# Kernel optimization log

Hardware: AMD Instinct MI355X
Metric: run time of the kernel (lower is better)

## Reference

```python
import jax, jax.numpy as jnp
import numpy as np

B, T, D, H, Q = 8, 1024, 256, 4, 3
DK = D // H


def _ln(x, g, b):
    m = x.mean(-1, keepdims=True)
    v = x.var(-1, keepdims=True)
    return (x - m) / jnp.sqrt(v + 1e-5) * g + b


def _grn(x, f1w, f1b, f2w, f2b, gw, gb, lng, lnb):
    # GatedResidualNetwork (input_size == output_size, dropout in eval mode)
    eta1 = jax.nn.elu(x @ f1w.T + f1b)
    eta2 = eta1 @ f2w.T + f2b
    a = jax.nn.sigmoid(eta2 @ gw.T + gb) * eta2
    return _ln(x + a, lng, lnb)


def setup_inputs() -> dict:
    key = jax.random.key(0)
    ks = jax.random.split(key, 24)
    s = 0.02
    p = {}
    p['x'] = jax.random.normal(ks[0], (B, T, D), dtype=jnp.float32)
    # GRN 1 (temporal enrichment before attention)
    p['g1_f1w'] = jax.random.normal(ks[1], (D, D)) * s
    p['g1_f1b'] = jnp.zeros((D,))
    p['g1_f2w'] = jax.random.normal(ks[2], (D, D)) * s
    p['g1_f2b'] = jnp.zeros((D,))
    p['g1_gw'] = jax.random.normal(ks[3], (D, D)) * s
    p['g1_gb'] = jnp.zeros((D,))
    p['g1_lng'] = jnp.ones((D,))
    p['g1_lnb'] = jnp.zeros((D,))
    # Multi-head self-attention
    p['wq'] = jax.random.normal(ks[4], (D, D)) * s
    p['wk'] = jax.random.normal(ks[5], (D, D)) * s
    p['wv'] = jax.random.normal(ks[6], (D, D)) * s
    p['wo_w'] = jax.random.normal(ks[7], (D, D)) * s
    p['wo_b'] = jnp.zeros((D,))
    p['attn_lng'] = jnp.ones((D,))
    p['attn_lnb'] = jnp.zeros((D,))
    # GRN 2 (post-attention gating)
    p['g2_f1w'] = jax.random.normal(ks[8], (D, D)) * s
    p['g2_f1b'] = jnp.zeros((D,))
    p['g2_f2w'] = jax.random.normal(ks[9], (D, D)) * s
    p['g2_f2b'] = jnp.zeros((D,))
    p['g2_gw'] = jax.random.normal(ks[10], (D, D)) * s
    p['g2_gb'] = jnp.zeros((D,))
    p['g2_lng'] = jnp.ones((D,))
    p['g2_lnb'] = jnp.zeros((D,))
    # Quantile heads: Linear(D -> Q)
    p['qh_w'] = jax.random.normal(ks[11], (Q, D)) * s
    p['qh_b'] = jnp.zeros((Q,))
    return p


def reference(x, g1_f1w, g1_f1b, g1_f2w, g1_f2b, g1_gw, g1_gb, g1_lng, g1_lnb,
              wq, wk, wv, wo_w, wo_b, attn_lng, attn_lnb,
              g2_f1w, g2_f1b, g2_f2w, g2_f2b, g2_gw, g2_gb, g2_lng, g2_lnb,
              qh_w, qh_b):
    b, t, d = x.shape
    h = _grn(x, g1_f1w, g1_f1b, g1_f2w, g1_f2b, g1_gw, g1_gb, g1_lng, g1_lnb)
    # self-attention (W_q/W_k/W_v have no bias, per module)
    q = (h @ wq.T).reshape(b, t, H, DK)
    k = (h @ wk.T).reshape(b, t, H, DK)
    v = (h @ wv.T).reshape(b, t, H, DK)
    scale = 1.0 / np.sqrt(DK).astype(np.float32)
    scores = jnp.einsum('bthd,bshd->bhts', q, k) * scale  # [B,H,T,T]
    attn = jax.nn.softmax(scores, axis=-1)
    ctx = jnp.einsum('bhts,bshd->bthd', attn, v).reshape(b, t, d)
    attn_out = ctx @ wo_w.T + wo_b
    h2 = _ln(h + attn_out, attn_lng, attn_lnb)
    h3 = _grn(h2, g2_f1w, g2_f1b, g2_f2w, g2_f2b, g2_gw, g2_gb, g2_lng, g2_lnb)
    # quantile heads on the last decoder step (CUDAQuantileHeadsFunction: [B,D]->[B,Q])
    out = h3[:, -1, :] @ qh_w.T + qh_b  # [B, Q]
    return out
```

## Files before the change

### kernel.cpp

```cpp
#include <hip/hip_runtime.h>
#include <hip/hip_bf16.h>
#include <math.h>

#define DD 256
#define BB 8
#define TT 1024
#define MM (BB*TT)
#define NH 4
#define DKH 64
#define NQ 3

typedef __attribute__((ext_vector_type(8))) short bf16x8;
typedef __attribute__((ext_vector_type(4))) float f32x4;
typedef unsigned short u16;
typedef unsigned int u32;

__device__ __forceinline__ float bf2f(u16 u) {
  return __uint_as_float(((u32)u) << 16);
}
__device__ __forceinline__ u16 f2bf(float x) {
  __hip_bfloat16 h = __float2bfloat16(x);
  return *reinterpret_cast<u16*>(&h);
}
__device__ __forceinline__ uint2 pack4(float a, float b, float c, float d) {
  uint2 r;
  r.x = (u32)f2bf(a) | ((u32)f2bf(b) << 16);
  r.y = (u32)f2bf(c) | ((u32)f2bf(d) << 16);
  return r;
}
__device__ __forceinline__ float wred(float v) {
#pragma unroll
  for (int off = 32; off; off >>= 1) v += __shfl_xor(v, off);
  return v;
}

#define NX8 (MM * DD / 8)
#define NW8 (65536 / 8)
#define NCHUNK (NX8 + 9 * NW8)

__global__ __launch_bounds__(256) void precast(
    const float* __restrict__ x,
    const float* __restrict__ w0, const float* __restrict__ w1,
    const float* __restrict__ w2, const float* __restrict__ w3,
    const float* __restrict__ w4, const float* __restrict__ w5,
    const float* __restrict__ w6, const float* __restrict__ w7,
    const float* __restrict__ w8_, u16* __restrict__ wb,
    u16* __restrict__ xb)
{
  const int c = blockIdx.x * 256 + threadIdx.x;
  if (c >= NCHUNK) return;
  const float* src;
  u16* dst;
  int off;
  if (c < NX8) {
    src = x; dst = xb; off = c * 8;
  } else {
    const int r = c - NX8;
    const int mi = r / NW8;
    off = (r - mi * NW8) * 8;
    switch (mi) {
      case 0: src = w0; break; case 1: src = w1; break;
      case 2: src = w2; break; case 3: src = w3; break;
      case 4: src = w4; break; case 5: src = w5; break;
      case 6: src = w6; break; case 7: src = w7; break;
      default: src = w8_; break;
    }
    dst = wb + mi * 65536;
  }
  const float4 v0 = *(const float4*)(src + off);
  const float4 v1 = *(const float4*)(src + off + 4);
  *(uint2*)(dst + off)     = pack4(v0.x, v0.y, v0.z, v0.w);
  *(uint2*)(dst + off + 4) = pack4(v1.x, v1.y, v1.z, v1.w);
}

template<int ACT>
__global__ __launch_bounds__(256) void gemm64(const u16* __restrict__ A_,
                                              const u16* __restrict__ W,
                                              const float* __restrict__ bias,
                                              u16* __restrict__ out)
{
  __shared__ u16 As[64][264];
  __shared__ u16 Bs[64][264];
  const int tid  = threadIdx.x;
  const int lane = tid & 63, wave = tid >> 6;
  const int wr = wave >> 1, wc = wave & 1;
  const int q  = lane >> 4, lr = lane & 15;
  const int m0 = blockIdx.x * 64, n0 = blockIdx.y * 64;

#pragma unroll
  for (int p = 0; p < 8; ++p) {
    const int c = tid + p * 256;
    const int row = c >> 5, col = (c & 31) * 8;
    *(uint4*)&As[row][col] = *(const uint4*)(A_ + (size_t)(m0 + row) * DD + col);
    *(uint4*)&Bs[row][col] = *(const uint4*)(W  + (size_t)(n0 + row) * DD + col);
  }
  __syncthreads();

  f32x4 acc[2][2] = {};
#pragma unroll
  for (int kk = 0; kk < 8; ++kk) {
    const int koff = kk * 32 + q * 8;
    bf16x8 av[2], bv[2];
    av[0] = *(const bf16x8*)&As[wr * 32 + lr][koff];
    av[1] = *(const bf16x8*)&As[wr * 32 + 16 + lr][koff];
    bv[0] = *(const bf16x8*)&Bs[wc * 32 + lr][koff];
    bv[1] = *(const bf16x8*)&Bs[wc * 32 + 16 + lr][koff];
#pragma unroll
    for (int i = 0; i < 2; ++i)
#pragma unroll
      for (int j = 0; j < 2; ++j)
        acc[i][j] = __builtin_amdgcn_mfma_f32_16x16x32_bf16(av[i], bv[j], acc[i][j], 0, 0, 0);
  }

#pragma unroll
  for (int i = 0; i < 2; ++i) {
#pragma unroll
    for (int j = 0; j < 2; ++j) {
      const int col = n0 + wc * 32 + j * 16 + lr;
      const float bvv = bias ? bias[col] : 0.f;
#pragma unroll
      for (int t = 0; t < 4; ++t) {
        const int row = m0 + wr * 32 + i * 16 + q * 4 + t;
        float v = acc[i][j][t] + bvv;
        if (ACT == 1) v = v > 0.f ? v : expm1f(v);
        out[(size_t)row * DD + col] = f2bf(v);
      }
    }
  }
}

__global__ __launch_bounds__(256) void gemm_kv(const u16* __restrict__ A_,
                                               const u16* __restrict__ Wk,
                                               const u16* __restrict__ Wv,
                                               u16* __restrict__ kout,
                                               u16* __restrict__ vout)
{
  __shared__ u16 As[64][264];
  __shared__ u16 Bs[64][264];
  const int tid  = threadIdx.x;
  const int lane = tid & 63, wave = tid >> 6;
  const int wr = wave >> 1, wc = wave & 1;
  const int q  = lane >> 4, lr = lane & 15;
  const int ny = blockIdx.y;
  const u16* W = (ny < 4) ? Wk : Wv;
  u16* out = (ny < 4) ? kout : vout;
  const int m0 = blockIdx.x * 64, n0 = (ny & 3) * 64;

#pragma unroll
  for (int p = 0; p < 8; ++p) {
    const int c = tid + p * 256;
    const int row = c >> 5, col = (c & 31) * 8;
    *(uint4*)&As[row][col] = *(const uint4*)(A_ + (size_t)(m0 + row) * DD + col);
    *(uint4*)&Bs[row][col] = *(const uint4*)(W  + (size_t)(n0 + row) * DD + col);
  }
  __syncthreads();

  f32x4 acc[2][2] = {};
#pragma unroll
  for (int kk = 0; kk < 8; ++kk) {
    const int koff = kk * 32 + q * 8;
    bf16x8 av[2], bv[2];
    av[0] = *(const bf16x8*)&As[wr * 32 + lr][koff];
    av[1] = *(const bf16x8*)&As[wr * 32 + 16 + lr][koff];
    bv[0] = *(const bf16x8*)&Bs[wc * 32 + lr][koff];
    bv[1] = *(const bf16x8*)&Bs[wc * 32 + 16 + lr][koff];
#pragma unroll
    for (int i = 0; i < 2; ++i)
#pragma unroll
      for (int j = 0; j < 2; ++j)
        acc[i][j] = __builtin_amdgcn_mfma_f32_16x16x32_bf16(av[i], bv[j], acc[i][j], 0, 0, 0);
  }

#pragma unroll
  for (int i = 0; i < 2; ++i) {
#pragma unroll
    for (int j = 0; j < 2; ++j) {
      const int col = n0 + wc * 32 + j * 16 + lr;
#pragma unroll
      for (int t = 0; t < 4; ++t) {
        const int row = m0 + wr * 32 + i * 16 + q * 4 + t;
        out[(size_t)row * DD + col] = f2bf(acc[i][j][t]);
      }
    }
  }
}

__global__ __launch_bounds__(256) void grn_gate_ln(
    const u16* __restrict__ eta2, const u16* __restrict__ W,
    const float* __restrict__ gb, const float* __restrict__ x,
    const float* __restrict__ lng, const float* __restrict__ lnb,
    u16* __restrict__ hout, float* __restrict__ hlast)
{
  __shared__ u16 As[32][136];
  __shared__ u16 Bs[256][136];
  __shared__ float red_s[32][5];
  __shared__ float red_q[32][5];
  __shared__ float smean[32], srstd[32];

  const int tid  = threadIdx.x;
  const int lane = tid & 63, wave = tid >> 6;
  const int q  = lane >> 4, lr = lane & 15;
  const int m0 = blockIdx.x * 32;

  f32x4 acc[2][4] = {};

  for (int k0 = 0; k0 < DD; k0 += 128) {
#pragma unroll
    for (int p = 0; p < 2; ++p) {
      const int c = tid + p * 256;
      const int row = c >> 4, col = (c & 15) * 8;
      *(uint4*)&As[row][col] = *(const uint4*)(eta2 + (size_t)(m0 + row) * DD + k0 + col);
    }
#pragma unroll
    for (int p = 0; p < 16; ++p) {
      const int c = tid + p * 256;
      const int row = c >> 4, col = (c & 15) * 8;
      *(uint4*)&Bs[row][col] = *(const uint4*)(W + (size_t)row * DD + k0 + col);
    }
    __syncthreads();
#pragma unroll
    for (int kk = 0; kk < 4; ++kk) {
      const int koff = kk * 32 + q * 8;
      bf16x8 av[2], bv[4];
#pragma unroll
      for (int i = 0; i < 2; ++i) av[i] = *(const bf16x8*)&As[i * 16 + lr][koff];
#pragma unroll
      for (int j = 0; j < 4; ++j) bv[j] = *(const bf16x8*)&Bs[wave * 64 + j * 16 + lr][koff];
#pragma unroll
      for (int i = 0; i < 2; ++i)
#pragma unroll
        for (int j = 0; j < 4; ++j)
          acc[i][j] = __builtin_amdgcn_mfma_f32_16x16x32_bf16(av[i], bv[j], acc[i][j], 0, 0, 0);
    }
    __syncthreads();
  }

  float pre[2][4][4];
#pragma unroll
  for (int i = 0; i < 2; ++i) {
#pragma unroll
    for (int j = 0; j < 4; ++j) {
      const int n = wave * 64 + j * 16 + lr;
      const float gbn = gb[n];
#pragma unroll
      for (int t = 0; t < 4; ++t) {
        const int grow = m0 + i * 16 + q * 4 + t;
        const float gate = acc[i][j][t] + gbn;
        const float sig = 1.f / (1.f + expf(-gate));
        const float e2 = bf2f(eta2[(size_t)grow * DD + n]);
        pre[i][j][t] = x[(size_t)grow * DD + n] + sig * e2;
      }
    }
  }
#pragma unroll
  for (int i = 0; i < 2; ++i) {
#pragma unroll
    for (int t = 0; t < 4; ++t) {
      float s = 0.f, sq = 0.f;
#pragma unroll
      for (int j = 0; j < 4; ++j) { const float v = pre[i][j][t]; s += v; sq += v * v; }
#pragma unroll
      for (int m = 1; m <= 8; m <<= 1) { s += __shfl_xor(s, m); sq += __shfl_xor(sq, m); }
      if (lr == 0) {
        const int ml = i * 16 + q * 4 + t;
        red_s[ml][wave] = s;
        red_q[ml][wave] = sq;
      }
    }
  }
  __syncthreads();
  if (tid < 32) {
    const float s  = red_s[tid][0] + red_s[tid][1] + red_s[tid][2] + red_s[tid][3];
    const float sq = red_q[tid][0] + red_q[tid][1] + red_q[tid][2] + red_q[tid][3];
    const float mean = s * (1.f / DD);
    const float var = sq * (1.f / DD) - mean * mean;
    smean[tid] = mean;
    srstd[tid] = rsqrtf(var + 1e-5f);
  }
  __syncthreads();
#pragma unroll
  for (int i = 0; i < 2; ++i) {
#pragma unroll
    for (int j = 0; j < 4; ++j) {
      const int n = wave * 64 + j * 16 + lr;
      const float gn = lng[n], bn = lnb[n];
#pragma unroll
      for (int t = 0; t < 4; ++t) {
        const int ml = i * 16 + q * 4 + t;
        const int grow = m0 + ml;
        const float hn = (pre[i][j][t] - smean[ml]) * srstd[ml] * gn + bn;
        hout[(size_t)grow * DD + n] = f2bf(hn);
        if ((grow & (TT - 1)) == (TT - 1))
          hlast[(size_t)(grow >> 10) * DD + n] = hn;
      }
    }
  }
}

__global__ __launch_bounds__(256) void qk_softmax_ctx(
    const float* __restrict__ hlast, const u16* __restrict__ kbuf,
    const u16* __restrict__ vbuf, const float* __restrict__ wq,
    float* __restrict__ ctxbuf)
{
  __shared__ float hl[DD], qh[DKH];
  __shared__ float red[8];
  __shared__ float pr[TT];
  __shared__ float part[8][DKH];
  const int h = blockIdx.x, b = blockIdx.y;
  const int tid = threadIdx.x, lane = tid & 63, w = tid >> 6;

  hl[tid] = hlast[(size_t)b * DD + tid];
  __syncthreads();
  {
    const int j = tid >> 2, seg = tid & 3;
    const float* wr = wq + (size_t)(h * DKH + j) * DD + seg * 64;
    const float* sp = hl + seg * 64;
    float acc = 0.f;
#pragma unroll
    for (int k = 0; k < 64; k += 4) {
      const float4 w4 = *(const float4*)(wr + k);
      acc += w4.x * sp[k] + w4.y * sp[k + 1] + w4.z * sp[k + 2] + w4.w * sp[k + 3];
    }
    acc += __shfl_xor(acc, 1);
    acc += __shfl_xor(acc, 2);
    if (seg == 0) qh[j] = acc;
  }
  __syncthreads();

  float sv[4], mx = -3.0e38f;
#pragma unroll
  for (int i = 0; i < 4; ++i) {
    const int s = tid + 256 * i;
    const u16* kr = kbuf + ((size_t)(b * TT + s)) * DD + h * DKH;
    float acc = 0.f;
#pragma unroll
    for (int d = 0; d < DKH; d += 8) {
      const bf16x8 kv = *(const bf16x8*)(kr + d);
#pragma unroll
      for (int e = 0; e < 8; ++e) acc += bf2f((u16)kv[e]) * qh[d + e];
    }
    sv[i] = acc * 0.125f;
    mx = fmaxf(mx, sv[i]);
  }
#pragma unroll
  for (int off = 32; off; off >>= 1) mx = fmaxf(mx, __shfl_xor(mx, off));
  if (lane == 0) red[w] = mx;
  __syncthreads();
  mx = fmaxf(fmaxf(red[0], red[1]), fmaxf(red[2], red[3]));
  float sum = 0.f;
#pragma unroll
  for (int i = 0; i < 4; ++i) { sv[i] = expf(sv[i] - mx); sum += sv[i]; }
  sum = wred(sum);
  if (lane == 0) red[4 + w] = sum;
  __syncthreads();
  const float inv = 1.f / (red[4] + red[5] + red[6] + red[7]);
#pragma unroll
  for (int i = 0; i < 4; ++i) pr[tid + 256 * i] = sv[i] * inv;
  __syncthreads();

  {
    const int np = (tid & 31) * 2, sg = tid >> 5;
    const u16* vp = vbuf + ((size_t)(b * TT + sg * 128)) * DD + h * DKH + np;
    const float* pp = pr + sg * 128;
    float a0 = 0.f, a1 = 0.f;
    for (int s = 0; s < 128; ++s) {
      const u32 vv = *(const u32*)(vp + (size_t)s * DD);
      const float p = pp[s];
      a0 += p * bf2f((u16)(vv & 0xffffu));
      a1 += p * bf2f((u16)(vv >> 16));
    }
    part[sg][np] = a0; part[sg][np + 1] = a1;
  }
  __syncthreads();
  if (tid < DKH) {
    float s = 0.f;
#pragma unroll
    for (int g = 0; g < 8; ++g) s += part[g][tid];
    ctxbuf[(size_t)b * DD + h * DKH + tid] = s;
  }
}

__device__ __forceinline__ void mv256b(const u16* __restrict__ W16,
                                       const float* __restrict__ srcbuf,
                                       float* __restrict__ dst,
                                       int wave, int lane)
{
  const int half = lane >> 5, l32 = lane & 31;
  float s[8];
  {
    const float4 s0 = *(const float4*)(srcbuf + l32 * 8);
    const float4 s1 = *(const float4*)(srcbuf + l32 * 8 + 4);
    s[0] = s0.x; s[1] = s0.y; s[2] = s0.z; s[3] = s0.w;
    s[4] = s1.x; s[5] = s1.y; s[6] = s1.z; s[7] = s1.w;
  }
#pragma unroll
  for (int i = 0; i < 8; ++i) {
    const int r = wave * 16 + i * 2 + half;
    const bf16x8 wv = *(const bf16x8*)(W16 + (size_t)r * DD + l32 * 8);
    float acc = 0.f;
#pragma unroll
    for (int e = 0; e < 8; ++e) acc += bf2f((u16)wv[e]) * s[e];
#pragma unroll
    for (int off = 16; off; off >>= 1) acc += __shfl_xor(acc, off);
    if (l32 == 0) dst[r] = acc;
  }
}

#define LN_STEP(val, gam, bet, dst) \
  __syncthreads(); \
  if (tid < DD) { lnS[tid] = (val); lnQ[tid] = (val) * (val); } \
  __syncthreads(); \
  if (tid < 64) { \
    float s_ = 0.f, q_ = 0.f; \
    _Pragma("unroll") \
    for (int i_ = 0; i_ < 4; ++i_) { s_ += lnS[tid + 64 * i_]; q_ += lnQ[tid + 64 * i_]; } \
    s_ = wred(s_); q_ = wred(q_); \
    if (tid == 0) { const float m_ = s_ * (1.f / DD); red2[0] = m_; red2[1] = rsqrtf(q_ * (1.f / DD) - m_ * m_ + 1e-5f); } \
  } \
  __syncthreads(); \
  if (tid < DD) dst[tid] = ((val) - red2[0]) * red2[1] * gam[tid] + bet[tid]; \
  __syncthreads();

__global__ __launch_bounds__(1024) void tail2(
    const float* __restrict__ hlast, const float* __restrict__ ctxbuf,
    const u16* __restrict__ wbf,
    const float* __restrict__ wob, const float* __restrict__ alng, const float* __restrict__ alnb,
    const float* __restrict__ f1b, const float* __restrict__ f2b,
    const float* __restrict__ gbv, const float* __restrict__ lng, const float* __restrict__ lnb,
    const float* __restrict__ qhw, const float* __restrict__ qhb,
    float* __restrict__ out)
{
  __shared__ float hl[DD], bufA[DD], bufB[DD], bufC[DD], part0[DD];
  __shared__ float lnS[DD], lnQ[DD];
  __shared__ float red2[2];
  const int b = blockIdx.x, tid = threadIdx.x;
  const int wave = tid >> 6, lane = tid & 63;

  if (tid < DD) {
    hl[tid]   = hlast[(size_t)b * DD + tid];
    bufB[tid] = ctxbuf[(size_t)b * DD + tid];
  }
  __syncthreads();

  mv256b(wbf + 0 * 65536, bufB, part0, wave, lane);
  __syncthreads();
  float v = 0.f;
  if (tid < DD) v = hl[tid] + part0[tid] + wob[tid];
  LN_STEP(v, alng, alnb, bufA)

  mv256b(wbf + 1 * 65536, bufA, part0, wave, lane);
  __syncthreads();
  if (tid < DD) {
    const float e1 = part0[tid] + f1b[tid];
    bufB[tid] = e1 > 0.f ? e1 : expm1f(e1);
  }
  __syncthreads();

  mv256b(wbf + 2 * 65536, bufB, part0, wave, lane);
  __syncthreads();
  if (tid < DD) bufC[tid] = part0[tid] + f2b[tid];
  __syncthreads();

  mv256b(wbf + 3 * 65536, bufC, part0, wave, lane);
  __syncthreads();
  v = 0.f;
  if (tid < DD) {
    const float g = part0[tid] + gbv[tid];
    v = bufA[tid] + (1.f / (1.f + expf(-g))) * bufC[tid];
  }
  LN_STEP(v, lng, lnb, bufA)

  if (tid < 64 * NQ) {
    const int qi = tid >> 6, l = tid & 63;
    float acc = 0.f;
#pragma unroll
    for (int i = 0; i < 4; ++i) acc += qhw[(size_t)qi * DD + l + 64 * i] * bufA[l + 64 * i];
    acc = wred(acc);
    if (l == 0) out[b * NQ + qi] = acc + qhb[qi];
  }
}

extern "C" void kernel_launch(void* const* d_in, const int* in_sizes, int n_in,
                              void* d_out, int out_size, void* d_ws, size_t ws_size,
                              hipStream_t stream)
{
  const float* x       = (const float*)d_in[0];
  const float* g1_f1w  = (const float*)d_in[1];
  const float* g1_f1b  = (const float*)d_in[2];
  const float* g1_f2w  = (const float*)d_in[3];
  const float* g1_f2b  = (const float*)d_in[4];
  const float* g1_gw   = (const float*)d_in[5];
  const float* g1_gb   = (const float*)d_in[6];
  const float* g1_lng  = (const float*)d_in[7];
  const float* g1_lnb  = (const float*)d_in[8];
  const float* wq      = (const float*)d_in[9];
  const float* wk      = (const float*)d_in[10];
  const float* wv      = (const float*)d_in[11];
  const float* wo_w    = (const float*)d_in[12];
  const float* wo_b    = (const float*)d_in[13];
  const float* attn_lng= (const float*)d_in[14];
  const float* attn_lnb= (const float*)d_in[15];
  const float* g2_f1w  = (const float*)d_in[16];
  const float* g2_f1b  = (const float*)d_in[17];
  const float* g2_f2w  = (const float*)d_in[18];
  const float* g2_f2b  = (const float*)d_in[19];
  const float* g2_gw   = (const float*)d_in[20];
  const float* g2_gb   = (const float*)d_in[21];
  const float* g2_lng  = (const float*)d_in[22];
  const float* g2_lnb  = (const float*)d_in[23];
  const float* qh_w    = (const float*)d_in[24];
  const float* qh_b    = (const float*)d_in[25];
  float* out = (float*)d_out;

  char* w8 = (char*)d_ws;
  u16*  wb    = (u16*)(w8);
  u16*  xb    = (u16*)(w8 + ((size_t)2  << 20));
  u16*  eta1  = (u16*)(w8 + ((size_t)6  << 20));
  u16*  eta2  = (u16*)(w8 + ((size_t)10 << 20));
  u16*  hbuf  = (u16*)(w8 + ((size_t)14 << 20));
  u16*  kbuf  = (u16*)(w8 + ((size_t)18 << 20));
  u16*  vbuf  = (u16*)(w8 + ((size_t)22 << 20));
  float* hlast = (float*)(w8 + ((size_t)26 << 20));
  float* ctxbuf = (float*)(w8 + ((size_t)26 << 20) + (64 << 10));

  const dim3 blk(256);
  const dim3 g1(MM / 64, DD / 64);

  precast<<<dim3((NCHUNK + 255) / 256), blk, 0, stream>>>(
      x, g1_f1w, g1_f2w, g1_gw, wk, wv, wo_w, g2_f1w, g2_f2w, g2_gw, wb, xb);
  gemm64<1><<<g1, blk, 0, stream>>>(xb,   wb + 0 * 65536, g1_f1b, eta1);
  gemm64<0><<<g1, blk, 0, stream>>>(eta1, wb + 1 * 65536, g1_f2b, eta2);
  grn_gate_ln<<<dim3(MM / 32), blk, 0, stream>>>(eta2, wb + 2 * 65536, g1_gb, x,
                                                 g1_lng, g1_lnb, hbuf, hlast);
  gemm_kv<<<dim3(MM / 64, 8), blk, 0, stream>>>(hbuf, wb + 3 * 65536, wb + 4 * 65536,
                                                kbuf, vbuf);
  qk_softmax_ctx<<<dim3(NH, BB), blk, 0, stream>>>(hlast, kbuf, vbuf, wq, ctxbuf);
  tail2<<<dim3(BB), dim3(1024), 0, stream>>>(hlast, ctxbuf, wb + 5 * 65536,
                                             wo_b, attn_lng, attn_lnb,
                                             g2_f1b, g2_f2b, g2_gb, g2_lng, g2_lnb,
                                             qh_w, qh_b, out);
}
```

Measured before the change: 77.32 us.

## Fuse GRN1 GEMM chain and K/V projections into one row-block kernel

Replaces the separate f1, f2, gate+LayerNorm and K/V GEMM kernels with a single kernel per 64-row block. It keeps intermediate activations (eta1, eta2, h) in shared memory and streams the 20 weight chunks through a register-prefetched buffer. The x-to-bf16 precast moves into the fused kernel. This removes the global round-trips for eta1, eta2, xb and h along with several kernel launches. In exchange it uses only 128 blocks with heavy LDS use, which lowers occupancy and parallelism, and each block streams all weights serially.

Result: slower. 116.2 us (+50.3%).

```diff
diff --git a/kernel.cpp b/kernel.cpp
--- a/kernel.cpp
+++ b/kernel.cpp
@@ -34,267 +34,255 @@
   return v;
 }
 
-#define NX8 (MM * DD / 8)
 #define NW8 (65536 / 8)
-#define NCHUNK (NX8 + 9 * NW8)
+#define NCHUNK (9 * NW8)
 
 __global__ __launch_bounds__(256) void precast(
-    const float* __restrict__ x,
     const float* __restrict__ w0, const float* __restrict__ w1,
     const float* __restrict__ w2, const float* __restrict__ w3,
     const float* __restrict__ w4, const float* __restrict__ w5,
     const float* __restrict__ w6, const float* __restrict__ w7,
-    const float* __restrict__ w8_, u16* __restrict__ wb,
-    u16* __restrict__ xb)
+    const float* __restrict__ w8_, u16* __restrict__ wb)
 {
   const int c = blockIdx.x * 256 + threadIdx.x;
   if (c >= NCHUNK) return;
+  const int mi = c / NW8;
+  const int off = (c - mi * NW8) * 8;
   const float* src;
-  u16* dst;
-  int off;
-  if (c < NX8) {
-    src = x; dst = xb; off = c * 8;
-  } else {
-    const int r = c - NX8;
-    const int mi = r / NW8;
-    off = (r - mi * NW8) * 8;
-    switch (mi) {
-      case 0: src = w0; break; case 1: src = w1; break;
-      case 2: src = w2; break; case 3: src = w3; break;
-      case 4: src = w4; break; case 5: src = w5; break;
-      case 6: src = w6; break; case 7: src = w7; break;
-      default: src = w8_; break;
-    }
-    dst = wb + mi * 65536;
-  }
+  switch (mi) {
+    case 0: src = w0; break; case 1: src = w1; break;
+    case 2: src = w2; break; case 3: src = w3; break;
+    case 4: src = w4; break; case 5: src = w5; break;
+    case 6: src = w6; break; case 7: src = w7; break;
+    default: src = w8_; break;
+  }
+  u16* dst = wb + mi * 65536;
   const float4 v0 = *(const float4*)(src + off);
   const float4 v1 = *(const float4*)(src + off + 4);
   *(uint2*)(dst + off)     = pack4(v0.x, v0.y, v0.z, v0.w);
   *(uint2*)(dst + off + 4) = pack4(v1.x, v1.y, v1.z, v1.w);
 }
 
-template<int ACT>
-__global__ __launch_bounds__(256) void gemm64(const u16* __restrict__ A_,
-                                              const u16* __restrict__ W,
-                                              const float* __restrict__ bias,
-                                              u16* __restrict__ out)
+__global__ __launch_bounds__(256) void mega(
+    const float* __restrict__ x, const u16* __restrict__ wb,
+    const float* __restrict__ f1b, const float* __restrict__ f2b,
+    const float* __restrict__ gb, const float* __restrict__ lng,
+    const float* __restrict__ lnb,
+    u16* __restrict__ kout, u16* __restrict__ vout,
+    float* __restrict__ hlast)
 {
-  __shared__ u16 As[64][264];
-  __shared__ u16 Bs[64][264];
+  __shared__ u16 bufA[64][264];
+  __shared__ u16 bufB[64][264];
+  __shared__ u16 Ws[64][264];
+  __shared__ float red_s[64][2];
+  __shared__ float red_q[64][2];
+  __shared__ float smean[64], srstd[64];
+
   const int tid  = threadIdx.x;
   const int lane = tid & 63, wave = tid >> 6;
   const int wr = wave >> 1, wc = wave & 1;
   const int q  = lane >> 4, lr = lane & 15;
-  const int m0 = blockIdx.x * 64, n0 = blockIdx.y * 64;
-
+  const int r0 = blockIdx.x * 64;
+
+  uint4 wreg[8];
+
+#define LOADW(w_) { \
+  const u16* wp_ = wb + (size_t)((w_) >> 2) * 65536 + ((w_) & 3) * 16384; \
+  _Pragma("unroll") \
+  for (int p = 0; p < 8; ++p) wreg[p] = *(const uint4*)(wp_ + (p * 256 + tid) * 8); }
+
+#define STOREW() { \
+  _Pragma("unroll") \
+  for (int p = 0; p < 8; ++p) { \
+    const int e_ = (p * 256 + tid) * 8; \
+    *(uint4*)&Ws[e_ >> 8][e_ & 255] = wreg[p]; } }
+
+#define ADVANCE() { __syncthreads(); STOREW(); if (w + 2 < 20) LOADW(w + 2); __syncthreads(); }
+
+#define MFMA_CHUNK(ABUF) \
+  _Pragma("unroll") \
+  for (int kk = 0; kk < 8; ++kk) { \
+    const int koff = kk * 32 + q * 8; \
+    const bf16x8 a0 = *(const bf16x8*)&ABUF[wr * 32 + lr][koff]; \
+    const bf16x8 a1 = *(const bf16x8*)&ABUF[wr * 32 + 16 + lr][koff]; \
+    const bf16x8 b0 = *(const bf16x8*)&Ws[wc * 32 + lr][koff]; \
+    const bf16x8 b1 = *(const bf16x8*)&Ws[wc * 32 + 16 + lr][koff]; \
+    acc[0][0] = __builtin_amdgcn_mfma_f32_16x16x32_bf16(a0, b0, acc[0][0], 0, 0, 0); \
+    acc[0][1] = __builtin_amdgcn_mfma_f32_16x16x32_bf16(a0, b1, acc[0][1], 0, 0, 0); \
+    acc[1][0] = __builtin_amdgcn_mfma_f32_16x16x32_bf16(a1, b0, acc[1][0], 0, 0, 0); \
+    acc[1][1] = __builtin_amdgcn_mfma_f32_16x16x32_bf16(a1, b1, acc[1][1], 0, 0, 0); \
+  }
+
+  LOADW(0);
 #pragma unroll
   for (int p = 0; p < 8; ++p) {
-    const int c = tid + p * 256;
-    const int row = c >> 5, col = (c & 31) * 8;
-    *(uint4*)&As[row][col] = *(const uint4*)(A_ + (size_t)(m0 + row) * DD + col);
-    *(uint4*)&Bs[row][col] = *(const uint4*)(W  + (size_t)(n0 + row) * DD + col);
-  }
-  __syncthreads();
-
-  f32x4 acc[2][2] = {};
-#pragma unroll
-  for (int kk = 0; kk < 8; ++kk) {
-    const int koff = kk * 32 + q * 8;
-    bf16x8 av[2], bv[2];
-    av[0] = *(const bf16x8*)&As[wr * 32 + lr][koff];
-    av[1] = *(const bf16x8*)&As[wr * 32 + 16 + lr][koff];
-    bv[0] = *(const bf16x8*)&Bs[wc * 32 + lr][koff];
-    bv[1] = *(const bf16x8*)&Bs[wc * 32 + 16 + lr][koff];
-#pragma unroll
-    for (int i = 0; i < 2; ++i)
-#pragma unroll
-      for (int j = 0; j < 2; ++j)
-        acc[i][j] = __builtin_amdgcn_mfma_f32_16x16x32_bf16(av[i], bv[j], acc[i][j], 0, 0, 0);
-  }
-
-#pragma unroll
-  for (int i = 0; i < 2; ++i) {
-#pragma unroll
-    for (int j = 0; j < 2; ++j) {
-      const int col = n0 + wc * 32 + j * 16 + lr;
-      const float bvv = bias ? bias[col] : 0.f;
-#pragma unroll
-      for (int t = 0; t < 4; ++t) {
-        const int row = m0 + wr * 32 + i * 16 + q * 4 + t;
-        float v = acc[i][j][t] + bvv;
-        if (ACT == 1) v = v > 0.f ? v : expm1f(v);
-        out[(size_t)row * DD + col] = f2bf(v);
-      }
-    }
-  }
-}
-
-__global__ __launch_bounds__(256) void gemm_kv(const u16* __restrict__ A_,
-                                               const u16* __restrict__ Wk,
-                                               const u16* __restrict__ Wv,
-                                               u16* __restrict__ kout,
-                                               u16* __restrict__ vout)
-{
-  __shared__ u16 As[64][264];
-  __shared__ u16 Bs[64][264];
-  const int tid  = threadIdx.x;
-  const int lane = tid & 63, wave = tid >> 6;
-  const int wr = wave >> 1, wc = wave & 1;
-  const int q  = lane >> 4, lr = lane & 15;
-  const int ny = blockIdx.y;
-  const u16* W = (ny < 4) ? Wk : Wv;
-  u16* out = (ny < 4) ? kout : vout;
-  const int m0 = blockIdx.x * 64, n0 = (ny & 3) * 64;
-
-#pragma unroll
-  for (int p = 0; p < 8; ++p) {
-    const int c = tid + p * 256;
-    const int row = c >> 5, col = (c & 31) * 8;
-    *(uint4*)&As[row][col] = *(const uint4*)(A_ + (size_t)(m0 + row) * DD + col);
-    *(uint4*)&Bs[row][col] = *(const uint4*)(W  + (size_t)(n0 + row) * DD + col);
-  }
-  __syncthreads();
-
-  f32x4 acc[2][2] = {};
-#pragma unroll
-  for (int kk = 0; kk < 8; ++kk) {
-    const int koff = kk * 32 + q * 8;
-    bf16x8 av[2], bv[2];
-    av[0] = *(const bf16x8*)&As[wr * 32 + lr][koff];
-    av[1] = *(const bf16x8*)&As[wr * 32 + 16 + lr][koff];
-    bv[0] = *(const bf16x8*)&Bs[wc * 32 + lr][koff];
-    bv[1] = *(const bf16x8*)&Bs[wc * 32 + 16 + lr][koff];
-#pragma unroll
-    for (int i = 0; i < 2; ++i)
-#pragma unroll
-      for (int j = 0; j < 2; ++j)
-        acc[i][j] = __builtin_amdgcn_mfma_f32_16x16x32_bf16(av[i], bv[j], acc[i][j], 0, 0, 0);
-  }
-
-#pragma unroll
-  for (int i = 0; i < 2; ++i) {
-#pragma unroll
-    for (int j = 0; j < 2; ++j) {
-      const int col = n0 + wc * 32 + j * 16 + lr;
-#pragma unroll
-      for (int t = 0; t < 4; ++t) {
-        const int row = m0 + wr * 32 + i * 16 + q * 4 + t;
-        out[(size_t)row * DD + col] = f2bf(acc[i][j][t]);
-      }
-    }
-  }
-}
-
-__global__ __launch_bounds__(256) void grn_gate_ln(
-    const u16* __restrict__ eta2, const u16* __restrict__ W,
-    const float* __restrict__ gb, const float* __restrict__ x,
-    const float* __restrict__ lng, const float* __restrict__ lnb,
-    u16* __restrict__ hout, float* __restrict__ hlast)
-{
-  __shared__ u16 As[32][136];
-  __shared__ u16 Bs[256][136];
-  __shared__ float red_s[32][5];
-  __shared__ float red_q[32][5];
-  __shared__ float smean[32], srstd[32];
-
-  const int tid  = threadIdx.x;
-  const int lane = tid & 63, wave = tid >> 6;
-  const int q  = lane >> 4, lr = lane & 15;
-  const int m0 = blockIdx.x * 32;
-
-  f32x4 acc[2][4] = {};
-
-  for (int k0 = 0; k0 < DD; k0 += 128) {
-#pragma unroll
-    for (int p = 0; p < 2; ++p) {
-      const int c = tid + p * 256;
-      const int row = c >> 4, col = (c & 15) * 8;
-      *(uint4*)&As[row][col] = *(const uint4*)(eta2 + (size_t)(m0 + row) * DD + k0 + col);
-    }
-#pragma unroll
-    for (int p = 0; p < 16; ++p) {
-      const int c = tid + p * 256;
-      const int row = c >> 4, col = (c & 15) * 8;
-      *(uint4*)&Bs[row][col] = *(const uint4*)(W + (size_t)row * DD + k0 + col);
-    }
-    __syncthreads();
-#pragma unroll
-    for (int kk = 0; kk < 4; ++kk) {
-      const int koff = kk * 32 + q * 8;
-      bf16x8 av[2], bv[4];
-#pragma unroll
-      for (int i = 0; i < 2; ++i) av[i] = *(const bf16x8*)&As[i * 16 + lr][koff];
-#pragma unroll
-      for (int j = 0; j < 4; ++j) bv[j] = *(const bf16x8*)&Bs[wave * 64 + j * 16 + lr][koff];
-#pragma unroll
-      for (int i = 0; i < 2; ++i)
-#pragma unroll
-        for (int j = 0; j < 4; ++j)
-          acc[i][j] = __builtin_amdgcn_mfma_f32_16x16x32_bf16(av[i], bv[j], acc[i][j], 0, 0, 0);
-    }
-    __syncthreads();
-  }
-
-  float pre[2][4][4];
-#pragma unroll
-  for (int i = 0; i < 2; ++i) {
-#pragma unroll
-    for (int j = 0; j < 4; ++j) {
-      const int n = wave * 64 + j * 16 + lr;
-      const float gbn = gb[n];
-#pragma unroll
-      for (int t = 0; t < 4; ++t) {
-        const int grow = m0 + i * 16 + q * 4 + t;
-        const float gate = acc[i][j][t] + gbn;
-        const float sig = 1.f / (1.f + expf(-gate));
-        const float e2 = bf2f(eta2[(size_t)grow * DD + n]);
-        pre[i][j][t] = x[(size_t)grow * DD + n] + sig * e2;
-      }
-    }
-  }
-#pragma unroll
-  for (int i = 0; i < 2; ++i) {
+    const int e = (p * 256 + tid) * 8;
+    const int row = e >> 8, col = e & 255;
+    const float* xp = x + (size_t)(r0 + row) * DD + col;
+    const float4 v0 = *(const float4*)xp;
+    const float4 v1 = *(const float4*)(xp + 4);
+    *(uint2*)&bufA[row][col]     = pack4(v0.x, v0.y, v0.z, v0.w);
+    *(uint2*)&bufA[row][col + 4] = pack4(v1.x, v1.y, v1.z, v1.w);
+  }
+  __syncthreads();
+  STOREW();
+  LOADW(1);
+  __syncthreads();
+
+  int w = 0;
+  float rs[2][4] = {{0}}, rq[2][4] = {{0}};
+
+  for (int nc = 0; nc < 4; ++nc, ++w) {
+    f32x4 acc[2][2] = {};
+    MFMA_CHUNK(bufA);
+#pragma unroll
+    for (int i = 0; i < 2; ++i)
+#pragma unroll
+      for (int j = 0; j < 2; ++j) {
+        const int col = nc * 64 + wc * 32 + j * 16 + lr;
+        const float bias = f1b[col];
+#pragma unroll
+        for (int t = 0; t < 4; ++t) {
+          const int row = wr * 32 + i * 16 + q * 4 + t;
+          float v = acc[i][j][t] + bias;
+          v = v > 0.f ? v : expm1f(v);
+          bufB[row][col] = f2bf(v);
+        }
+      }
+    ADVANCE();
+  }
+
+  for (int nc = 0; nc < 4; ++nc, ++w) {
+    f32x4 acc[2][2] = {};
+    MFMA_CHUNK(bufB);
+#pragma unroll
+    for (int i = 0; i < 2; ++i)
+#pragma unroll
+      for (int j = 0; j < 2; ++j) {
+        const int col = nc * 64 + wc * 32 + j * 16 + lr;
+        const float bias = f2b[col];
+#pragma unroll
+        for (int t = 0; t < 4; ++t) {
+          const int row = wr * 32 + i * 16 + q * 4 + t;
+          bufA[row][col] = f2bf(acc[i][j][t] + bias);
+        }
+      }
+    ADVANCE();
+  }
+
+  for (int nc = 0; nc < 4; ++nc, ++w) {
+    float xr[2][2][4];
+#pragma unroll
+    for (int i = 0; i < 2; ++i)
+#pragma unroll
+      for (int j = 0; j < 2; ++j) {
+        const int col = nc * 64 + wc * 32 + j * 16 + lr;
+#pragma unroll
+        for (int t = 0; t < 4; ++t)
+          xr[i][j][t] = x[(size_t)(r0 + wr * 32 + i * 16 + q * 4 + t) * DD + col];
+      }
+    f32x4 acc[2][2] = {};
+    MFMA_CHUNK(bufA);
+#pragma unroll
+    for (int i = 0; i < 2; ++i)
+#pragma unroll
+      for (int j = 0; j < 2; ++j) {
+        const int col = nc * 64 + wc * 32 + j * 16 + lr;
+        const float gbn = gb[col];
+#pragma unroll
+        for (int t = 0; t < 4; ++t) {
+          const int row = wr * 32 + i * 16 + q * 4 + t;
+          const float gate = acc[i][j][t] + gbn;
+          const float sig = 1.f / (1.f + expf(-gate));
+          const float e2 = bf2f(bufA[row][col]);
+          const float pre = xr[i][j][t] + sig * e2;
+          rs[i][t] += pre;
+          rq[i][t] += pre * pre;
+          bufB[row][col] = f2bf(pre);
+        }
+      }
+    ADVANCE();
+  }
+
+#pragma unroll
+  for (int i = 0; i < 2; ++i)
 #pragma unroll
     for (int t = 0; t < 4; ++t) {
-      float s = 0.f, sq = 0.f;
-#pragma unroll
-      for (int j = 0; j < 4; ++j) { const float v = pre[i][j][t]; s += v; sq += v * v; }
+      float s = rs[i][t], sq = rq[i][t];
 #pragma unroll
       for (int m = 1; m <= 8; m <<= 1) { s += __shfl_xor(s, m); sq += __shfl_xor(sq, m); }
       if (lr == 0) {
-        const int ml = i * 16 + q * 4 + t;
-        red_s[ml][wave] = s;
-        red_q[ml][wave] = sq;
+        const int row = wr * 32 + i * 16 + q * 4 + t;
+        red_s[row][wc] = s;
+        red_q[row][wc] = sq;
       }
     }
-  }
-  __syncthreads();
-  if (tid < 32) {
-    const float s  = red_s[tid][0] + red_s[tid][1] + red_s[tid][2] + red_s[tid][3];
-    const float sq = red_q[tid][0] + red_q[tid][1] + red_q[tid][2] + red_q[tid][3];
+  __syncthreads();
+  if (tid < 64) {
+    const float s  = red_s[tid][0] + red_s[tid][1];
+    const float sq = red_q[tid][0] + red_q[tid][1];
     const float mean = s * (1.f / DD);
-    const float var = sq * (1.f / DD) - mean * mean;
     smean[tid] = mean;
-    srstd[tid] = rsqrtf(var + 1e-5f);
-  }
-  __syncthreads();
-#pragma unroll
-  for (int i = 0; i < 2; ++i) {
-#pragma unroll
-    for (int j = 0; j < 4; ++j) {
-      const int n = wave * 64 + j * 16 + lr;
-      const float gn = lng[n], bn = lnb[n];
-#pragma unroll
-      for (int t = 0; t < 4; ++t) {
-        const int ml = i * 16 + q * 4 + t;
-        const int grow = m0 + ml;
-        const float hn = (pre[i][j][t] - smean[ml]) * srstd[ml] * gn + bn;
-        hout[(size_t)grow * DD + n] = f2bf(hn);
-        if ((grow & (TT - 1)) == (TT - 1))
-          hlast[(size_t)(grow >> 10) * DD + n] = hn;
-      }
-    }
-  }
+    srstd[tid] = rsqrtf(sq * (1.f / DD) - mean * mean + 1e-5f);
+  }
+  __syncthreads();
+  const bool lastblk = ((r0 + 63) & (TT - 1)) == (TT - 1);
+#pragma unroll
+  for (int nc = 0; nc < 4; ++nc)
+#pragma unroll
+    for (int i = 0; i < 2; ++i)
+#pragma unroll
+      for (int j = 0; j < 2; ++j) {
+        const int col = nc * 64 + wc * 32 + j * 16 + lr;
+        const float gn = lng[col], bn = lnb[col];
+#pragma unroll
+        for (int t = 0; t < 4; ++t) {
+          const int row = wr * 32 + i * 16 + q * 4 + t;
+          const float h = (bf2f(bufB[row][col]) - smean[row]) * srstd[row] * gn + bn;
+          bufB[row][col] = f2bf(h);
+          if (lastblk && row == 63)
+            hlast[(size_t)(r0 >> 10) * DD + col] = h;
+        }
+      }
+  __syncthreads();
+
+  for (int nc = 0; nc < 4; ++nc, ++w) {
+    f32x4 acc[2][2] = {};
+    MFMA_CHUNK(bufB);
+#pragma unroll
+    for (int i = 0; i < 2; ++i)
+#pragma unroll
+      for (int j = 0; j < 2; ++j) {
+        const int col = nc * 64 + wc * 32 + j * 16 + lr;
+#pragma unroll
+        for (int t = 0; t < 4; ++t) {
+          const int row = wr * 32 + i * 16 + q * 4 + t;
+          kout[(size_t)(r0 + row) * DD + col] = f2bf(acc[i][j][t]);
+        }
+      }
+    ADVANCE();
+  }
+
+  for (int nc = 0; nc < 4; ++nc, ++w) {
+    f32x4 acc[2][2] = {};
+    MFMA_CHUNK(bufB);
+#pragma unroll
+    for (int i = 0; i < 2; ++i)
+#pragma unroll
+      for (int j = 0; j < 2; ++j) {
+        const int col = nc * 64 + wc * 32 + j * 16 + lr;
+#pragma unroll
+        for (int t = 0; t < 4; ++t) {
+          const int row = wr * 32 + i * 16 + q * 4 + t;
+          vout[(size_t)(r0 + row) * DD + col] = f2bf(acc[i][j][t]);
+        }
+      }
+    if (w < 19) ADVANCE();
+  }
+#undef LOADW
+#undef STOREW
+#undef ADVANCE
+#undef MFMA_CHUNK
 }
 
 __global__ __launch_bounds__(256) void qk_softmax_ctx(
@@ -514,26 +502,17 @@
 
   char* w8 = (char*)d_ws;
   u16*  wb    = (u16*)(w8);
-  u16*  xb    = (u16*)(w8 + ((size_t)2  << 20));
-  u16*  eta1  = (u16*)(w8 + ((size_t)6  << 20));
-  u16*  eta2  = (u16*)(w8 + ((size_t)10 << 20));
-  u16*  hbuf  = (u16*)(w8 + ((size_t)14 << 20));
-  u16*  kbuf  = (u16*)(w8 + ((size_t)18 << 20));
-  u16*  vbuf  = (u16*)(w8 + ((size_t)22 << 20));
-  float* hlast = (float*)(w8 + ((size_t)26 << 20));
-  float* ctxbuf = (float*)(w8 + ((size_t)26 << 20) + (64 << 10));
+  u16*  kbuf  = (u16*)(w8 + ((size_t)2  << 20));
+  u16*  vbuf  = (u16*)(w8 + ((size_t)6  << 20));
+  float* hlast  = (float*)(w8 + ((size_t)10 << 20));
+  float* ctxbuf = (float*)(w8 + ((size_t)10 << 20) + (64 << 10));
 
   const dim3 blk(256);
-  const dim3 g1(MM / 64, DD / 64);
 
   precast<<<dim3((NCHUNK + 255) / 256), blk, 0, stream>>>(
-      x, g1_f1w, g1_f2w, g1_gw, wk, wv, wo_w, g2_f1w, g2_f2w, g2_gw, wb, xb);
-  gemm64<1><<<g1, blk, 0, stream>>>(xb,   wb + 0 * 65536, g1_f1b, eta1);
-  gemm64<0><<<g1, blk, 0, stream>>>(eta1, wb + 1 * 65536, g1_f2b, eta2);
-  grn_gate_ln<<<dim3(MM / 32), blk, 0, stream>>>(eta2, wb + 2 * 65536, g1_gb, x,
-                                                 g1_lng, g1_lnb, hbuf, hlast);
-  gemm_kv<<<dim3(MM / 64, 8), blk, 0, stream>>>(hbuf, wb + 3 * 65536, wb + 4 * 65536,
-                                                kbuf, vbuf);
+      g1_f1w, g1_f2w, g1_gw, wk, wv, wo_w, g2_f1w, g2_f2w, g2_gw, wb);
+  mega<<<dim3(MM / 64), blk, 0, stream>>>(x, wb, g1_f1b, g1_f2b, g1_gb,
+                                          g1_lng, g1_lnb, kbuf, vbuf, hlast);
   qk_softmax_ctx<<<dim3(NH, BB), blk, 0, stream>>>(hlast, kbuf, vbuf, wq, ctxbuf);
   tail2<<<dim3(BB), dim3(1024), 0, stream>>>(hlast, ctxbuf, wb + 5 * 65536,
                                              wo_b, attn_lng, attn_lnb,
```
